# Kernel tuning notes

Hardware: AMD Instinct MI355X
Metric: run time of the kernel (lower is better)

## Reference

```python
import jax, jax.numpy as jnp
import numpy as np

B, T, IN, H = 512, 1024, 1, 64


def setup_inputs() -> dict:
    key = jax.random.key(0)
    ks = jax.random.split(key, 7)
    s = 1.0 / np.sqrt(H)  # PyTorch LSTM init range
    u = lambda k, shape: jax.random.uniform(k, shape, jnp.float32, -s, s)
    return {
        "x": jax.random.normal(ks[0], (B, T, IN), jnp.float32),
        "W_ih": u(ks[1], (4 * H, IN)),
        "W_hh": u(ks[2], (4 * H, H)),
        "b_ih": u(ks[3], (4 * H,)),
        "b_hh": u(ks[4], (4 * H,)),
        "W_lin": u(ks[5], (1, H)),
        "b_lin": u(ks[6], (1,)),
    }


def reference(x, W_ih, W_hh, b_ih, b_hh, W_lin, b_lin):
    # x: [B, T, IN] (batch_first). Identity quantizers => plain LSTM math.
    Bsz = x.shape[0]
    Hs = W_hh.shape[1]
    bias = b_ih + b_hh  # fold the two bias vectors once
    xs = jnp.swapaxes(x, 0, 1)  # [T, B, IN] for scan over time
    h0 = jnp.zeros((Bsz, Hs), x.dtype)
    c0 = jnp.zeros((Bsz, Hs), x.dtype)

    def step(carry, xt):
        h, c = carry
        gates = xt @ W_ih.T + h @ W_hh.T + bias  # [B, 4H]
        i, f, g, o = jnp.split(gates, 4, axis=-1)  # PyTorch gate order i,f,g,o
        i = jax.nn.sigmoid(i)
        f = jax.nn.sigmoid(f)
        g = jnp.tanh(g)
        o = jax.nn.sigmoid(o)
        c_new = f * c + i * g
        h_new = o * jnp.tanh(c_new)
        return (h_new, c_new), None

    (h_final, _), _ = jax.lax.scan(step, (h0, c0), xs)
    # final_hidden_states.squeeze(0) -> [B, H]; linear -> [B, 1]; view(-1) -> [B]
    return (h_final @ W_lin.T + b_lin).reshape(-1)
```

## Files before the change

### kernel.cpp

```cpp
#include <hip/hip_runtime.h>


#define TLEN 1024
#define HID  64

__device__ __forceinline__ float fast_sigmoid(float x) {
    return __builtin_amdgcn_rcpf(1.0f + __expf(-x));
}
__device__ __forceinline__ float fast_tanh(float x) {
    return __builtin_fmaf(2.0f, fast_sigmoid(2.0f * x), -1.0f);
}

__global__ __launch_bounds__(256, 2)
void qlstm_kernel(const float* __restrict__ x,
                  const float* __restrict__ W_ih,
                  const float* __restrict__ W_hh,
                  const float* __restrict__ b_ih,
                  const float* __restrict__ b_hh,
                  const float* __restrict__ W_lin,
                  const float* __restrict__ b_lin,
                  float* __restrict__ out)
{
    const int b   = blockIdx.x;
    const int tid = threadIdx.x;
    const int w   = tid >> 6;
    const int l   = tid & 63;

    __shared__ __align__(16) float xs[TLEN];
    __shared__ __align__(16) float hs4[4][HID];
    __shared__ __align__(16) float act[2][4][HID];

    ((float4*)xs)[tid] = ((const float4*)(x + (size_t)b * TLEN))[tid];

    const int row = w * HID + l;
    const float4* Wr = (const float4*)(W_hh + (size_t)row * HID);
    float4 wq[16];
    #pragma unroll
    for (int q = 0; q < 16; ++q) wq[q] = Wr[q];

    const float u    = W_ih[row];
    const float bias = b_ih[row] + b_hh[row];
    const float wlin = W_lin[l];

    float c = 0.0f, h = 0.0f;
    hs4[w][l] = 0.0f;
    __syncthreads();

    for (int t = 0; t < TLEN; ++t) {
        const int p = t & 1;
        const float xt = xs[t];

        float acc = __builtin_fmaf(xt, u, bias);
        #pragma unroll
        for (int q = 0; q < 16; ++q) {
            const float4 hk = *(const float4*)&hs4[w][4 * q];
            acc = __builtin_fmaf(hk.x, wq[q].x, acc);
            acc = __builtin_fmaf(hk.y, wq[q].y, acc);
            acc = __builtin_fmaf(hk.z, wq[q].z, acc);
            acc = __builtin_fmaf(hk.w, wq[q].w, acc);
        }

        const float a = (w == 2) ? fast_tanh(acc) : fast_sigmoid(acc);
        act[p][w][l] = a;
        __syncthreads();

        const float ai = act[p][0][l];
        const float af = act[p][1][l];
        const float ag = act[p][2][l];
        const float ao = act[p][3][l];
        c = __builtin_fmaf(af, c, ai * ag);
        h = ao * fast_tanh(c);
        hs4[w][l] = h;
    }

    if (w == 0) {
        float v = h * wlin;
        #pragma unroll
        for (int off = 32; off > 0; off >>= 1)
            v += __shfl_down(v, off, 64);
        if (l == 0) out[b] = v + b_lin[0];
    }
}

extern "C" void kernel_launch(void* const* d_in, const int* in_sizes, int n_in,
                              void* d_out, int out_size, void* d_ws, size_t ws_size,
                              hipStream_t stream) {
    const float* x     = (const float*)d_in[0];
    const float* W_ih  = (const float*)d_in[1];
    const float* W_hh  = (const float*)d_in[2];
    const float* b_ih  = (const float*)d_in[3];
    const float* b_hh  = (const float*)d_in[4];
    const float* W_lin = (const float*)d_in[5];
    const float* b_lin = (const float*)d_in[6];
    float* out = (float*)d_out;

    const int B = out_size;
    qlstm_kernel<<<B, 256, 0, stream>>>(x, W_ih, W_hh, b_ih, b_hh, W_lin, b_lin, out);
}
```

Measured before the change: 586.6 us.

## Split hidden-dot product across two wave halves per gate with partial-sum exchange

Doubles the block to 512 threads so each gate row's 64-wide recurrent dot product is split into two 32-element halves computed by separate waves. Partial sums go through shared memory, and every wave then redundantly adds the halves and applies all four gate activations itself. This halves the serial FMA chain per timestep and the W_hh registers held per thread. In exchange it raises the thread count per block, adds redundant transcendental work in every wave, and keeps one barrier per step across eight waves instead of four.

Result: slower. 680.8 us (+16.1%).

```diff
diff --git a/kernel.cpp b/kernel.cpp
--- a/kernel.cpp
+++ b/kernel.cpp
@@ -11,7 +11,7 @@
     return __builtin_fmaf(2.0f, fast_sigmoid(2.0f * x), -1.0f);
 }
 
-__global__ __launch_bounds__(256, 2)
+__global__ __launch_bounds__(512, 4)
 void qlstm_kernel(const float* __restrict__ x,
                   const float* __restrict__ W_ih,
                   const float* __restrict__ W_hh,
@@ -21,56 +21,62 @@
                   const float* __restrict__ b_lin,
                   float* __restrict__ out)
 {
-    const int b   = blockIdx.x;
-    const int tid = threadIdx.x;
-    const int w   = tid >> 6;
-    const int l   = tid & 63;
+    const int b    = blockIdx.x;
+    const int tid  = threadIdx.x;
+    const int w    = tid >> 6;
+    const int g    = w & 3;
+    const int half = w >> 2;
+    const int l    = tid & 63;
 
     __shared__ __align__(16) float xs[TLEN];
-    __shared__ __align__(16) float hs4[4][HID];
-    __shared__ __align__(16) float act[2][4][HID];
+    __shared__ __align__(16) float hs[8][HID];
+    __shared__ __align__(16) float part[2][8][HID];
 
-    ((float4*)xs)[tid] = ((const float4*)(x + (size_t)b * TLEN))[tid];
+    ((float2*)xs)[tid] = ((const float2*)(x + (size_t)b * TLEN))[tid];
 
-    const int row = w * HID + l;
-    const float4* Wr = (const float4*)(W_hh + (size_t)row * HID);
-    float4 wq[16];
+    const int row = g * HID + l;
+    const float4* Wr = (const float4*)(W_hh + (size_t)row * HID + 32 * half);
+    float4 wq[8];
     #pragma unroll
-    for (int q = 0; q < 16; ++q) wq[q] = Wr[q];
+    for (int q = 0; q < 8; ++q) wq[q] = Wr[q];
 
     const float u    = W_ih[row];
     const float bias = b_ih[row] + b_hh[row];
     const float wlin = W_lin[l];
 
     float c = 0.0f, h = 0.0f;
-    hs4[w][l] = 0.0f;
+    hs[w][l] = 0.0f;
     __syncthreads();
+
+    const float* hsw = &hs[w][32 * half];
 
     for (int t = 0; t < TLEN; ++t) {
         const int p = t & 1;
         const float xt = xs[t];
 
-        float acc = __builtin_fmaf(xt, u, bias);
+        float acc = (half == 0) ? __builtin_fmaf(xt, u, bias) : 0.0f;
         #pragma unroll
-        for (int q = 0; q < 16; ++q) {
-            const float4 hk = *(const float4*)&hs4[w][4 * q];
+        for (int q = 0; q < 8; ++q) {
+            const float4 hk = *(const float4*)&hsw[4 * q];
             acc = __builtin_fmaf(hk.x, wq[q].x, acc);
             acc = __builtin_fmaf(hk.y, wq[q].y, acc);
             acc = __builtin_fmaf(hk.z, wq[q].z, acc);
             acc = __builtin_fmaf(hk.w, wq[q].w, acc);
         }
-
-        const float a = (w == 2) ? fast_tanh(acc) : fast_sigmoid(acc);
-        act[p][w][l] = a;
+        part[p][w][l] = acc;
         __syncthreads();
 
-        const float ai = act[p][0][l];
-        const float af = act[p][1][l];
-        const float ag = act[p][2][l];
-        const float ao = act[p][3][l];
+        const float gi = part[p][0][l] + part[p][4][l];
+        const float gf = part[p][1][l] + part[p][5][l];
+        const float gg = part[p][2][l] + part[p][6][l];
+        const float go = part[p][3][l] + part[p][7][l];
+        const float ai = fast_sigmoid(gi);
+        const float af = fast_sigmoid(gf);
+        const float ag = fast_tanh(gg);
+        const float ao = fast_sigmoid(go);
         c = __builtin_fmaf(af, c, ai * ag);
         h = ao * fast_tanh(c);
-        hs4[w][l] = h;
+        hs[w][l] = h;
     }
 
     if (w == 0) {
@@ -95,5 +101,5 @@
     float* out = (float*)d_out;
 
     const int B = out_size;
-    qlstm_kernel<<<B, 256, 0, stream>>>(x, W_ih, W_hh, b_ih, b_hh, W_lin, b_lin, out);
+    qlstm_kernel<<<B, 512, 0, stream>>>(x, W_ih, W_hh, b_ih, b_hh, W_lin, b_lin, out);
 }
```

## Process two batch sequences per block to share weights and barriers

Applied to the files above, without the earlier changes.

Each 256-thread block now advances two independent batch sequences through the recurrence instead of one, so the grid is halved. Every W_hh element is used for two dot products, giving two independent FMA chains per thread and one barrier per timestep for both sequences. The weight row is now read through a pointer inside the time loop rather than preloaded into registers, and the occupancy hint in the launch bounds is dropped. The risks are fewer waves per CU to hide latency, and weight reloads per step if the compiler does not hoist them.

After: 840.6 us. 43.3% more time.

```diff
diff --git a/kernel.cpp b/kernel.cpp
--- a/kernel.cpp
+++ b/kernel.cpp
@@ -11,7 +11,7 @@
     return __builtin_fmaf(2.0f, fast_sigmoid(2.0f * x), -1.0f);
 }
 
-__global__ __launch_bounds__(256, 2)
+__global__ __launch_bounds__(256)
 void qlstm_kernel(const float* __restrict__ x,
                   const float* __restrict__ W_ih,
                   const float* __restrict__ W_hh,
@@ -21,64 +21,88 @@
                   const float* __restrict__ b_lin,
                   float* __restrict__ out)
 {
-    const int b   = blockIdx.x;
+    const int b0  = blockIdx.x * 2;
     const int tid = threadIdx.x;
     const int w   = tid >> 6;
     const int l   = tid & 63;
 
-    __shared__ __align__(16) float xs[TLEN];
-    __shared__ __align__(16) float hs4[4][HID];
-    __shared__ __align__(16) float act[2][4][HID];
+    __shared__ __align__(16) float xs[2][TLEN];
+    __shared__ __align__(16) float hs4[4][2][HID];
+    __shared__ __align__(16) float act[2][4][2][HID];
 
-    ((float4*)xs)[tid] = ((const float4*)(x + (size_t)b * TLEN))[tid];
+    {
+        const float4* src = (const float4*)(x + (size_t)b0 * TLEN);
+        float4* dst = (float4*)xs;
+        dst[tid]       = src[tid];
+        dst[tid + 256] = src[tid + 256];
+    }
 
     const int row = w * HID + l;
     const float4* Wr = (const float4*)(W_hh + (size_t)row * HID);
-    float4 wq[16];
-    #pragma unroll
-    for (int q = 0; q < 16; ++q) wq[q] = Wr[q];
 
     const float u    = W_ih[row];
     const float bias = b_ih[row] + b_hh[row];
     const float wlin = W_lin[l];
 
-    float c = 0.0f, h = 0.0f;
-    hs4[w][l] = 0.0f;
+    float c0 = 0.0f, h0 = 0.0f, c1 = 0.0f, h1 = 0.0f;
+    hs4[w][0][l] = 0.0f;
+    hs4[w][1][l] = 0.0f;
     __syncthreads();
 
     for (int t = 0; t < TLEN; ++t) {
         const int p = t & 1;
-        const float xt = xs[t];
+        const float xt0 = xs[0][t];
+        const float xt1 = xs[1][t];
 
-        float acc = __builtin_fmaf(xt, u, bias);
+        float acc0 = __builtin_fmaf(xt0, u, bias);
+        float acc1 = __builtin_fmaf(xt1, u, bias);
         #pragma unroll
         for (int q = 0; q < 16; ++q) {
-            const float4 hk = *(const float4*)&hs4[w][4 * q];
-            acc = __builtin_fmaf(hk.x, wq[q].x, acc);
-            acc = __builtin_fmaf(hk.y, wq[q].y, acc);
-            acc = __builtin_fmaf(hk.z, wq[q].z, acc);
-            acc = __builtin_fmaf(hk.w, wq[q].w, acc);
+            const float4 wv  = Wr[q];
+            const float4 hk0 = *(const float4*)&hs4[w][0][4 * q];
+            const float4 hk1 = *(const float4*)&hs4[w][1][4 * q];
+            acc0 = __builtin_fmaf(hk0.x, wv.x, acc0);
+            acc1 = __builtin_fmaf(hk1.x, wv.x, acc1);
+            acc0 = __builtin_fmaf(hk0.y, wv.y, acc0);
+            acc1 = __builtin_fmaf(hk1.y, wv.y, acc1);
+            acc0 = __builtin_fmaf(hk0.z, wv.z, acc0);
+            acc1 = __builtin_fmaf(hk1.z, wv.z, acc1);
+            acc0 = __builtin_fmaf(hk0.w, wv.w, acc0);
+            acc1 = __builtin_fmaf(hk1.w, wv.w, acc1);
         }
 
-        const float a = (w == 2) ? fast_tanh(acc) : fast_sigmoid(acc);
-        act[p][w][l] = a;
+        const float a0 = (w == 2) ? fast_tanh(acc0) : fast_sigmoid(acc0);
+        const float a1 = (w == 2) ? fast_tanh(acc1) : fast_sigmoid(acc1);
+        act[p][w][0][l] = a0;
+        act[p][w][1][l] = a1;
         __syncthreads();
 
-        const float ai = act[p][0][l];
-        const float af = act[p][1][l];
-        const float ag = act[p][2][l];
-        const float ao = act[p][3][l];
-        c = __builtin_fmaf(af, c, ai * ag);
-        h = ao * fast_tanh(c);
-        hs4[w][l] = h;
+        {
+            const float ai = act[p][0][0][l];
+            const float af = act[p][1][0][l];
+            const float ag = act[p][2][0][l];
+            const float ao = act[p][3][0][l];
+            c0 = __builtin_fmaf(af, c0, ai * ag);
+            h0 = ao * fast_tanh(c0);
+            hs4[w][0][l] = h0;
+        }
+        {
+            const float ai = act[p][0][1][l];
+            const float af = act[p][1][1][l];
+            const float ag = act[p][2][1][l];
+            const float ao = act[p][3][1][l];
+            c1 = __builtin_fmaf(af, c1, ai * ag);
+            h1 = ao * fast_tanh(c1);
+            hs4[w][1][l] = h1;
+        }
     }
 
-    if (w == 0) {
-        float v = h * wlin;
+    if (w == 0 || w == 1) {
+        float v = ((w == 0) ? h0 : h1) * wlin;
         #pragma unroll
         for (int off = 32; off > 0; off >>= 1)
             v += __shfl_down(v, off, 64);
-        if (l == 0) out[b] = v + b_lin[0];
+        if (l == 0) out[b0 + w] = v + b_lin[0];
     }
 }
 
@@ -95,5 +119,5 @@
     float* out = (float*)d_out;
 
     const int B = out_size;
-    qlstm_kernel<<<B, 256, 0, stream>>>(x, W_ih, W_hh, b_ih, b_hh, W_lin, b_lin, out);
+    qlstm_kernel<<<B / 2, 256, 0, stream>>>(x, W_ih, W_hh, b_ih, b_hh, W_lin, b_lin, out);
 }
```
